# Performance work log

Hardware: AMD Instinct MI355X
Metric: run time of the kernel (lower is better)

## Reference

```python
import jax, jax.numpy as jnp
import numpy as np

# 5x5 binomial (Gaussian) kernel, as in the swd-pytorch reference this repo vendors
_K = (np.outer([1, 4, 6, 4, 1], [1, 4, 6, 4, 1]) / 256.0).astype(np.float32)

SLICE = 7
N_DESC = 128
N_REPEAT = 128
PROJ_PER_REPEAT = 4


def _gauss_conv(x, stride):
    # depthwise 5x5 conv, padding=2, NCHW
    C = x.shape[1]
    k = jnp.broadcast_to(jnp.asarray(_K)[None, None], (C, 1, 5, 5)).astype(x.dtype)
    return jax.lax.conv_general_dilated(
        x, k, window_strides=(stride, stride), padding=[(2, 2), (2, 2)],
        dimension_numbers=('NCHW', 'OIHW', 'NCHW'), feature_group_count=C)


def _pyr_up(x):
    up = jnp.repeat(jnp.repeat(x, 2, axis=2), 2, axis=3)
    return _gauss_conv(up, 1)


def _laplacian_pyramid(x, n_pyramids):
    gauss = [x]
    for _ in range(n_pyramids):
        gauss.append(_gauss_conv(gauss[-1], 2))  # pyr_down
    lap = [gauss[i] - _pyr_up(gauss[i + 1]) for i in range(n_pyramids)]
    lap.append(gauss[-1])
    return lap


def _extract_patches(layer, rows, cols):
    # gather only the selected 7x7 patches instead of materializing the full unfold
    B, C = layer.shape[0], layer.shape[1]

    def one(r, c):
        return jax.lax.dynamic_slice(layer, (0, 0, r, c), (B, C, SLICE, SLICE))

    p = jax.vmap(one)(rows, cols)           # [n_desc, B, C, 7, 7]
    p = jnp.transpose(p, (1, 0, 2, 3, 4))   # [B, n_desc, C, 7, 7]
    mean = jnp.mean(p, axis=(0, 1, 3, 4), keepdims=True)
    std = jnp.std(p, axis=(0, 1, 3, 4), keepdims=True, ddof=1)  # torch.std is unbiased
    p = (p - mean) / (std + 1e-8)
    return p.reshape(-1, C * SLICE * SLICE)  # [B*n_desc, 147]


def _lap_swd(x, y):
    n_pyramids = int(np.rint(np.log2(x.shape[2] // 16)))
    pyr1 = _laplacian_pyramid(x, n_pyramids)
    pyr2 = _laplacian_pyramid(y, n_pyramids)
    key = jax.random.key(42)
    results = []
    for i, (l1, l2) in enumerate(zip(pyr1, pyr2)):
        H, W = l1.shape[2], l1.shape[3]
        n = (H - 6) * (W - 6)
        k_idx, k_proj = jax.random.split(jax.random.fold_in(key, i))
        idx = jax.random.permutation(k_idx, n)[:min(N_DESC, n)]
        rows, cols = idx // (W - 6), idx % (W - 6)
        p1 = _extract_patches(l1, rows, cols)
        p2 = _extract_patches(l2, rows, cols)
        D = p1.shape[1]
        # all 128 repeats x 4 projections batched into one [D, 512] matrix;
        # per-column std normalization == per-repeat normalization in the original
        rand = jax.random.normal(k_proj, (D, N_REPEAT * PROJ_PER_REPEAT), dtype=p1.dtype)
        rand = rand / jnp.std(rand, axis=0, keepdims=True, ddof=1)
        proj1 = jnp.sort(p1 @ rand, axis=0)
        proj2 = jnp.sort(p2 @ rand, axis=0)
        # mean over 128 repeats of mean(|d|) == global mean (equal group sizes)
        results.append(jnp.mean(jnp.abs(proj1 - proj2)))
    return jnp.mean(jnp.stack(results)) * 1000.0


def setup_inputs() -> dict:
    key = jax.random.key(0)
    kx, ky = jax.random.split(key)
    x = jax.random.normal(kx, (128, 3, 256, 256), dtype=jnp.float32)
    y = jax.random.normal(ky, (128, 3, 256, 256), dtype=jnp.float32)
    return {"x": x, "y": y}


def reference(x, y):
    return _lap_swd(x, y)
```

## Files before the change

### kernel.cpp

```cpp
#include <hip/hip_runtime.h>
#include <hip/hip_bf16.h>
#include <cstdint>
#include <cmath>
#include <vector>
#include <algorithm>
#include <numeric>


#define SIDX(i) ((i) ^ ((((i) >> 5) ^ ((i) >> 10)) & 31))
#define EXB 1024

typedef __attribute__((ext_vector_type(8))) short bf16x8;
typedef __attribute__((ext_vector_type(4))) float f32x4;
typedef __attribute__((ext_vector_type(4))) unsigned short us4;

struct RC { unsigned int rc[128]; };
struct Keys { uint32_t a[5]; uint32_t b[5]; };

__host__ __device__ inline void tf2x32(uint32_t k0, uint32_t k1,
                                       uint32_t x0, uint32_t x1,
                                       uint32_t& o0, uint32_t& o1) {
  uint32_t k2 = k0 ^ k1 ^ 0x1BD11BDAu;
  x0 += k0; x1 += k1;
#define TFR(r) { x0 += x1; x1 = (x1 << r) | (x1 >> (32 - r)); x1 ^= x0; }
  TFR(13) TFR(15) TFR(26) TFR(6)   x0 += k1; x1 += k2 + 1u;
  TFR(17) TFR(29) TFR(16) TFR(24)  x0 += k2; x1 += k0 + 2u;
  TFR(13) TFR(15) TFR(26) TFR(6)   x0 += k0; x1 += k1 + 3u;
  TFR(17) TFR(29) TFR(16) TFR(24)  x0 += k1; x1 += k2 + 4u;
  TFR(13) TFR(15) TFR(26) TFR(6)   x0 += k2; x1 += k0 + 5u;
#undef TFR
  o0 = x0; o1 = x1;
}

struct HostTables {
  RC rcs[5];
  uint32_t kp0[5], kp1[5];
  HostTables() {
    static const int Hs[5] = {256, 128, 64, 32, 16};
    for (int l = 0; l < 5; ++l) {
      uint32_t f0, f1;
      tf2x32(0u, 42u, 0u, (uint32_t)l, f0, f1);
      uint32_t ik0, ik1;
      tf2x32(f0, f1, 0u, 0u, ik0, ik1);
      tf2x32(f0, f1, 0u, 1u, kp0[l], kp1[l]);
      int Wm6 = Hs[l] - 6;
      int n = Wm6 * Wm6;
      int nd = n < 128 ? n : 128;
      std::vector<int> perm(n);
      std::iota(perm.begin(), perm.end(), 0);
      int rounds = (int)std::ceil(3.0 * std::log((double)n) / std::log(4294967295.0));
      uint32_t key0 = ik0, key1 = ik1;
      std::vector<uint32_t> bits(n);
      std::vector<int> ord(n), tmp(n);
      for (int r = 0; r < rounds; ++r) {
        uint32_t nk0, nk1, s0, s1;
        tf2x32(key0, key1, 0u, 0u, nk0, nk1);
        tf2x32(key0, key1, 0u, 1u, s0, s1);
        key0 = nk0; key1 = nk1;
        for (int tt = 0; tt < n; ++tt) {
          uint32_t o0, o1;
          tf2x32(s0, s1, 0u, (uint32_t)tt, o0, o1);
          bits[tt] = o0 ^ o1;
        }
        std::iota(ord.begin(), ord.end(), 0);
        std::stable_sort(ord.begin(), ord.end(),
                         [&](int A, int B) { return bits[A] < bits[B]; });
        for (int i2 = 0; i2 < n; ++i2) tmp[i2] = perm[ord[i2]];
        perm.swap(tmp);
      }
      for (int d = 0; d < 128; ++d) {
        int vv = (d < nd) ? perm[d] : 0;
        rcs[l].rc[d] = ((uint32_t)(vv / Wm6) << 16) | (uint32_t)(vv % Wm6);
      }
    }
  }
};
static const HostTables g_tbl;

__device__ inline float erfinv_f(float x) {
  float w = -log1pf(-x * x);
  float p;
  if (w < 5.0f) {
    w = w - 2.5f;
    p = 2.81022636e-08f;
    p = fmaf(p, w, 3.43273939e-07f);
    p = fmaf(p, w, -3.5233877e-06f);
    p = fmaf(p, w, -4.39150654e-06f);
    p = fmaf(p, w, 0.00021858087f);
    p = fmaf(p, w, -0.00125372503f);
    p = fmaf(p, w, -0.00417768164f);
    p = fmaf(p, w, 0.246640727f);
    p = fmaf(p, w, 1.50140941f);
  } else {
    w = sqrtf(w) - 3.0f;
    p = -0.000200214257f;
    p = fmaf(p, w, 0.000100950558f);
    p = fmaf(p, w, 0.00134934322f);
    p = fmaf(p, w, -0.00367342844f);
    p = fmaf(p, w, 0.00573950773f);
    p = fmaf(p, w, -0.0076224613f);
    p = fmaf(p, w, 0.00943887047f);
    p = fmaf(p, w, 1.00167406f);
    p = fmaf(p, w, 2.83297682f);
  }
  return p * x;
}

__device__ inline float bits_to_normal(uint32_t b) {
  union { uint32_t u; float f; } cv;
  cv.u = (b >> 9) | 0x3f800000u;
  float f = cv.f - 1.0f;
  const float lo = -0.99999994f;
  const float span = 1.0f - lo;
  float u = fmaxf(lo, __fadd_rn(__fmul_rn(f, span), lo));
  return 1.41421356237f * erfinv_f(u);
}

__device__ inline uint32_t pack_bf16x2(float v) {
  uint32_t u = __float_as_uint(v);
  uint32_t hi = (u + 0x7fffu + ((u >> 16) & 1u)) >> 16;
  float r = v - __uint_as_float(hi << 16);
  uint32_t ul = __float_as_uint(r);
  uint32_t lo = (ul + 0x7fffu + ((ul >> 16) & 1u)) >> 16;
  return hi | (lo << 16);
}


__global__ __launch_bounds__(256) void down_kernel(
    const float* __restrict__ inX, float* __restrict__ outX,
    const float* __restrict__ inY, float* __restrict__ outY,
    int H, int ltr, int lgW) {
  __shared__ __align__(16) float si[2816];
  __shared__ float hb[1408];
  int W = 1 << lgW;
  int lgWo = lgW - 1;
  int Wo = W >> 1, Ho = H >> 1;
  int TR = 1 << ltr;
  int lgnby = lgWo - ltr;
  int nby = 1 << lgnby;
  int per = 384 << lgnby;
  int bid = blockIdx.x;
  const float* in = inX; float* out = outX;
  if (bid >= per) { bid -= per; in = inY; out = outY; }
  int bc = bid >> lgnby;
  int by = bid & (nby - 1);
  int oy0 = by << ltr;
  int rows = 2 * TR + 3;
  int y0 = 2 * oy0 - 2;
  const float* src = in + (size_t)bc * H * W;
  int t = threadIdx.x;

  int nf4 = (rows << lgW) >> 2;
  for (int i = t; i < nf4; i += 256) {
    int fi = i << 2;
    int r = fi >> lgW, x = fi & (W - 1);
    int y = y0 + r;
    float4 v = (y >= 0 && y < H) ? *(const float4*)(src + ((size_t)y << lgW) + x)
                                 : make_float4(0.f, 0.f, 0.f, 0.f);
    *(float4*)(si + fi) = v;
  }
  __syncthreads();

  int nh = rows << lgWo;
  for (int i = t; i < nh; i += 256) {
    int r = i >> lgWo, ox = i & (Wo - 1);
    const float* rp = si + (r << lgW);
    int xb = 2 * ox;
    float s = 0.375f * rp[xb] + 0.25f * rp[xb + 1];
    if (ox >= 1) s += 0.0625f * rp[xb - 2] + 0.25f * rp[xb - 1];
    if (xb + 2 < W) s += 0.0625f * rp[xb + 2];
    hb[i] = s;
  }
  __syncthreads();

  int no = TR << lgWo;
  float* dst = out + (size_t)bc * Ho * Wo;
  for (int i = t; i < no; i += 256) {
    int r = i >> lgWo, ox = i & (Wo - 1);
    const float* cp = hb + ((2 * r) << lgWo) + ox;
    float s = 0.0625f * cp[0] + 0.25f * cp[Wo] + 0.375f * cp[2 * Wo] +
              0.25f * cp[3 * Wo] + 0.0625f * cp[4 * Wo];
    dst[((size_t)(oy0 + r) << lgWo) + ox] = s;
  }
}

__global__ void randgen_kernel(float* __restrict__ rnd, Keys ks,
                               float* __restrict__ misc) {
  int t = blockIdx.x * 256 + threadIdx.x;
  if (blockIdx.x == 0 && threadIdx.x < 128) misc[threadIdx.x] = 0.f;
  const int per = 75264;
  int l = t / per;
  int tt = t - l * per;
  if (l < 5) {
    uint32_t o0, o1;
    tf2x32(ks.a[l], ks.b[l], 0u, (uint32_t)tt, o0, o1);
    rnd[l * per + tt] = bits_to_normal(o0 ^ o1);
  }
}

__global__ void rndstats_kernel(const float* __restrict__ rnd,
                                float* __restrict__ inv1s,
                                float* __restrict__ scS) {
  int t = blockIdx.x * 256 + threadIdx.x;
  int l = t >> 9, j = t & 511;
  const float* rp = rnd + (size_t)l * 75264 + j;
  float sum = 0.f, q = 0.f;
  float sc[3];
#pragma unroll
  for (int c = 0; c < 3; ++c) {
    float s = 0.f;
    for (int ff = 0; ff < 49; ++ff) {
      float v = rp[(c * 49 + ff) * 512];
      s += v; q = fmaf(v, v, q);
    }
    sc[c] = s; sum += s;
  }
  float mean = sum * (1.f / 147.f);
  float var = (q - 147.f * mean * mean) * (1.f / 146.f);
  inv1s[t] = 1.f / sqrtf(var);
#pragma unroll
  for (int c = 0; c < 3; ++c) scS[(size_t)l * 1536 + c * 512 + j] = sc[c];
}

template <int PAR>
__device__ __forceinline__ void lap7(
    const float* __restrict__ gc, const float (&q0)[6], const float (&q1)[6],
    const float (&q2)[6], int cb, int H, float rw0, float rw2,
    uint32_t* __restrict__ po, float& sum7, float& sq7) {
#pragma unroll
  for (int v = 0; v < 7; ++v) {
    const int iw = ((v + PAR) >> 1) + 1;
    const int xo = PAR ^ (v & 1);
    int x = cb + v;
    float val = gc[x];
    float cw0 = (x >= 2) ? (xo ? 0.0625f : 0.3125f) : 0.f;
    float cw2 = (x <= H - 3) ? (xo ? 0.3125f : 0.0625f) : 0.f;
    float s0 = cw0 * q0[iw - 1] + 0.625f * q0[iw] + cw2 * q0[iw + 1];
    float s1 = cw0 * q1[iw - 1] + 0.625f * q1[iw] + cw2 * q1[iw + 1];
    float s2 = cw0 * q2[iw - 1] + 0.625f * q2[iw] + cw2 * q2[iw + 1];
    val -= rw0 * s0 + 0.625f * s1 + rw2 * s2;
    po[v] = pack_bf16x2(val);
    sum7 += val; sq7 = fmaf(val, val, sq7);
  }
}

__global__ __launch_bounds__(256) void extract_kernel(
    const float* __restrict__ g1, const float* __restrict__ gn1,
    uint32_t* __restrict__ p1g, float* __restrict__ part1,
    const float* __restrict__ g2, const float* __restrict__ gn2,
    uint32_t* __restrict__ p2g, float* __restrict__ part2,
    RC rcs, int H, int nd, int useLap, int M) {
  __shared__ float ls[6];
  if (threadIdx.x < 6) ls[threadIdx.x] = 0.f;
  __syncthreads();
  int half = (blockIdx.x >= EXB) ? 1 : 0;
  int bid = blockIdx.x - half * EXB;
  const float* g = half ? g2 : g1;
  const float* gn = half ? gn2 : gn1;
  uint32_t* p = half ? p2g : p1g;
  float* part = half ? part2 : part1;
  int totalU = M * 22;
  for (int unit = bid * 256 + threadIdx.x; unit < totalU; unit += EXB * 256) {
    int row = unit / 22;
    int k = unit - row * 22;
    if (k < 21) {
      int d, b;
      if (nd == 128) { d = row & 127; b = row >> 7; }
      else { b = row / nd; d = row - b * nd; }
      unsigned rc = rcs.rc[d];
      int r = (int)(rc >> 16);
      int cb = (int)(rc & 0xffffu);
      int c = k / 7, u = k - (k / 7) * 7;
      int y = r + u;
      const float* gc = g + ((size_t)(b * 3 + c)) * H * H + (size_t)y * H;
      uint32_t* po = p + (size_t)row * 160 + c * 49 + u * 7;
      float sum7 = 0.f, sq7 = 0.f;
      if (useLap) {
        int H2 = H >> 1;
        const float* gnc = gn + ((size_t)(b * 3 + c)) * H2 * H2;
        int h = y >> 1, yo = y & 1;
        float rw0 = (y >= 2) ? (yo ? 0.0625f : 0.3125f) : 0.f;
        float rw2 = (y <= H - 3) ? (yo ? 0.3125f : 0.0625f) : 0.f;
        int r0 = max(h - 1, 0), r2 = min(h + 1, H2 - 1);
        const float* R0 = gnc + (size_t)r0 * H2;
        const float* R1 = gnc + (size_t)h * H2;
        const float* R2 = gnc + (size_t)r2 * H2;
        int wb = (cb >> 1) - 1;
        float q0[6], q1[6], q2[6];
#pragma unroll
        for (int kk = 0; kk < 6; ++kk) {
          int a = wb + kk;
          a = a < 0 ? 0 : (a > H2 - 1 ? H2 - 1 : a);
          q0[kk] = R0[a]; q1[kk] = R1[a]; q2[kk] = R2[a];
        }
        if (cb & 1) lap7<1>(gc, q0, q1, q2, cb, H, rw0, rw2, po, sum7, sq7);
        else        lap7<0>(gc, q0, q1, q2, cb, H, rw0, rw2, po, sum7, sq7);
      } else {
#pragma unroll
        for (int v = 0; v < 7; ++v) {
          float val = gc[cb + v];
          po[v] = pack_bf16x2(val);
          sum7 += val; sq7 = fmaf(val, val, sq7);
        }
      }
      atomicAdd(&ls[c], sum7);
      atomicAdd(&ls[3 + c], sq7);
    } else {
      uint32_t* po = p + (size_t)row * 160 + 147;
      po[0] = 0x3F80u; po[1] = 0x3F80u; po[2] = 0x3F80u;
#pragma unroll
      for (int kk = 3; kk < 13; ++kk) po[kk] = 0u;
    }
  }
  __syncthreads();
  if (threadIdx.x < 6) part[bid * 6 + threadIdx.x] = ls[threadIdx.x];
}

__global__ void redpart_kernel(const float* __restrict__ part1,
                               const float* __restrict__ part2,
                               float* __restrict__ redg) {
  __shared__ float red[12];
  int tid = threadIdx.x;
  if (tid < 12) red[tid] = 0.f;
  __syncthreads();
  if (tid < 192) {
    int k = tid >> 4, r0 = tid & 15;
    const float* src = (k < 6) ? part1 : part2;
    int kk = (k < 6) ? k : k - 6;
    float ssum = 0.f;
    for (int r = r0; r < EXB; r += 16) ssum += src[r * 6 + kk];
    atomicAdd(&red[k], ssum);
  }
  __syncthreads();
  if (tid < 12) redg[tid] = red[tid];
}

__global__ void prep_kernel(
    const float* __restrict__ rnd, const float* __restrict__ inv1v,
    const float* __restrict__ scS, const float* __restrict__ redg,
    uint32_t* __restrict__ Bt1, uint32_t* __restrict__ Bt2, float Np) {
  int j = blockIdx.x;
  int f = threadIdx.x;
  if (f >= 160) return;
  int o = j * 160 + f;
  if (f >= 150) { Bt1[o] = 0u; Bt2[o] = 0u; return; }
  int c = (f < 147) ? (f / 49) : (f - 147);
  float m1 = redg[c] / Np;
  float v1 = (redg[3 + c] - Np * m1 * m1) / (Np - 1.f);
  float i1 = 1.f / (sqrtf(fmaxf(v1, 0.f)) + 1e-8f);
  float m2 = redg[6 + c] / Np;
  float v2 = (redg[9 + c] - Np * m2 * m2) / (Np - 1.f);
  float i2 = 1.f / (sqrtf(fmaxf(v2, 0.f)) + 1e-8f);
  float inv1 = inv1v[j];
  float w1, w2;
  if (f < 147) {
    float rv = rnd[f * 512 + j] * inv1;
    w1 = rv * i1; w2 = rv * i2;
  } else {
    float s = scS[c * 512 + j] * inv1;
    w1 = -m1 * i1 * s; w2 = -m2 * i2 * s;
  }
  Bt1[o] = pack_bf16x2(w1);
  Bt2[o] = pack_bf16x2(w2);
}

#define GBM 128
#define GBN 128
__global__ __launch_bounds__(256, 3) void gemm_kernel(
    const uint32_t* __restrict__ A1, const uint32_t* __restrict__ Bt1,
    const uint32_t* __restrict__ A2, const uint32_t* __restrict__ Bt2,
    float* __restrict__ C1, float* __restrict__ C2, int M) {
  __shared__ __align__(16) unsigned short AhS[128 * 40];
  __shared__ __align__(16) unsigned short AlS[128 * 40];
  __shared__ __align__(16) unsigned short BhS[128 * 40];
  __shared__ __align__(16) unsigned short BlS[128 * 40];
  int z = blockIdx.z;
  const uint32_t* A = z ? A2 : A1;
  const uint32_t* Bt = z ? Bt2 : Bt1;
  float* C = z ? C2 : C1;
  int bm = blockIdx.x * GBM;
  int bn = blockIdx.y * GBN;
  int tid = threadIdx.x;
  int lane = tid & 63;
  int wid = tid >> 6;
  int wm = wid & 1, wn = wid >> 1;
  int fr = lane & 15;
  int kb = (lane >> 4) << 3;
  f32x4 acc[4][4];
#pragma unroll
  for (int i = 0; i < 4; ++i)
#pragma unroll
    for (int j = 0; j < 4; ++j) acc[i][j] = (f32x4){0.f, 0.f, 0.f, 0.f};

  for (int k0 = 0; k0 < 160; k0 += 32) {
#pragma unroll
    for (int i = 0; i < 4; ++i) {
      int e = tid * 16 + i * 4;
      int m = e >> 5, kk = e & 31;
      uint4 v = *(const uint4*)(A + (size_t)(bm + m) * 160 + k0 + kk);
      us4 h = {(unsigned short)v.x, (unsigned short)v.y,
               (unsigned short)v.z, (unsigned short)v.w};
      us4 l = {(unsigned short)(v.x >> 16), (unsigned short)(v.y >> 16),
               (unsigned short)(v.z >> 16), (unsigned short)(v.w >> 16)};
      *(us4*)(AhS + m * 40 + kk) = h;
      *(us4*)(AlS + m * 40 + kk) = l;
      uint4 w = *(const uint4*)(Bt + (size_t)(bn + m) * 160 + k0 + kk);
      us4 wh = {(unsigned short)w.x, (unsigned short)w.y,
                (unsigned short)w.z, (unsigned short)w.w};
      us4 wl = {(unsigned short)(w.x >> 16), (unsigned short)(w.y >> 16),
                (unsigned short)(w.z >> 16), (unsigned short)(w.w >> 16)};
      *(us4*)(BhS + m * 40 + kk) = wh;
      *(us4*)(BlS + m * 40 + kk) = wl;
    }
    __syncthreads();
    bf16x8 ah[4], al[4], bh[4], bl[4];
#pragma unroll
    for (int mt = 0; mt < 4; ++mt) {
      int m = wm * 64 + mt * 16 + fr;
      ah[mt] = *(const bf16x8*)(AhS + m * 40 + kb);
      al[mt] = *(const bf16x8*)(AlS + m * 40 + kb);
    }
#pragma unroll
    for (int nt = 0; nt < 4; ++nt) {
      int n = wn * 64 + nt * 16 + fr;
      bh[nt] = *(const bf16x8*)(BhS + n * 40 + kb);
      bl[nt] = *(const bf16x8*)(BlS + n * 40 + kb);
    }
#pragma unroll
    for (int mt = 0; mt < 4; ++mt)
#pragma unroll
      for (int nt = 0; nt < 4; ++nt) {
        acc[mt][nt] = __builtin_amdgcn_mfma_f32_16x16x32_bf16(
            ah[mt], bh[nt], acc[mt][nt], 0, 0, 0);
        acc[mt][nt] = __builtin_amdgcn_mfma_f32_16x16x32_bf16(
            ah[mt], bl[nt], acc[mt][nt], 0, 0, 0);
        acc[mt][nt] = __builtin_amdgcn_mfma_f32_16x16x32_bf16(
            al[mt], bh[nt], acc[mt][nt], 0, 0, 0);
      }
    __syncthreads();
  }
  int mrow = (lane >> 4) << 2;
#pragma unroll
  for (int mt = 0; mt < 4; ++mt)
#pragma unroll
    for (int nt = 0; nt < 4; ++nt) {
      int n = bn + wn * 64 + nt * 16 + fr;
      int m = bm + wm * 64 + mt * 16 + mrow;
      f32x4 v = acc[mt][nt];
      *(float4*)(C + (size_t)n * 16384 + m) = make_float4(v[0], v[1], v[2], v[3]);
    }
}

__device__ inline int corank(const float* __restrict__ s, int pb, int L, int so) {
  int lo = so - L; lo = lo < 0 ? 0 : lo;
  int hi = so < L ? so : L;
  while (lo < hi) {
    int mid = (lo + hi) >> 1;
    float a = s[SIDX(pb + mid)];
    float b = s[SIDX(pb + L + so - 1 - mid)];
    if (a < b) lo = mid + 1; else hi = mid;
  }
  return lo;
}

__device__ __forceinline__ void merge_round(float (&v)[32], float* __restrict__ s,
                                            int t, int bi, int L, bool crosswave) {
  int sw = ((bi >> 5) ^ (bi >> 10)) & 31;
#pragma unroll
  for (int q = 0; q < 32; ++q) s[(bi + q) ^ sw] = v[q];
  if (crosswave) __syncthreads();
  else __builtin_amdgcn_wave_barrier();
  int pb = bi & ~(2 * L - 1);
  int so = bi - pb;
  int i0 = corank(s, pb, L, so);
  int nxt = __shfl_down(i0, 1, 64);
  int i1;
  if (((so + 32) & (2 * L - 1)) == 0) i1 = L;
  else if (crosswave && (t & 63) == 63) i1 = corank(s, pb, L, so + 32);
  else i1 = nxt;
  int na = i1 - i0;
  int j1 = so + 32 - i1;
#pragma unroll
  for (int q = 0; q < 32; ++q) {
    int idx = (q < na) ? (pb + i0 + q)
                       : (pb + L + j1 - 1 - (q - na));
    v[q] = s[SIDX(idx)];
  }
#pragma unroll
  for (int j = 16; j >= 1; j >>= 1) {
#pragma unroll
    for (int q = 0; q < 32; ++q) {
      if ((q & j) == 0) {
        float a = v[q], b = v[q | j];
        v[q] = fminf(a, b);
        v[q | j] = fmaxf(a, b);
      }
    }
  }
  if (crosswave) __syncthreads();
}

__device__ __forceinline__ void mergesort_col(float (&v)[32], float* __restrict__ s,
                                              int t, int bi) {
  for (int L = 32; L <= 1024; L <<= 1) merge_round(v, s, t, bi, L, false);
  for (int L = 2048; L <= 8192; L <<= 1) merge_round(v, s, t, bi, L, true);
}

__global__ __launch_bounds__(512, 4) void sortdiff_kernel(
    const float* __restrict__ proj1, const float* __restrict__ proj2,
    float* __restrict__ sum, int m) {
  __shared__ float s[16384];
  int t = threadIdx.x;
  int col = blockIdx.x;
  const float INF = __builtin_huge_valf();
  float va[32], vb[32];
  int bi = t << 5;

  const float* pa = proj1 + (size_t)col * 16384;
  const float* pbp = proj2 + (size_t)col * 16384;
  if (bi < m) {
#pragma unroll
    for (int i = 0; i < 8; ++i) {
      float4 A4 = *(const float4*)(pa + bi + i * 4);
      va[i * 4 + 0] = A4.x; va[i * 4 + 1] = A4.y;
      va[i * 4 + 2] = A4.z; va[i * 4 + 3] = A4.w;
      float4 B4 = *(const float4*)(pbp + bi + i * 4);
      vb[i * 4 + 0] = B4.x; vb[i * 4 + 1] = B4.y;
      vb[i * 4 + 2] = B4.z; vb[i * 4 + 3] = B4.w;
    }
  } else {
#pragma unroll
    for (int r = 0; r < 32; ++r) { va[r] = INF; vb[r] = INF; }
  }

#pragma unroll
  for (int k = 2; k <= 32; k <<= 1) {
#pragma unroll
    for (int j = k >> 1; j >= 1; j >>= 1) {
#pragma unroll
      for (int r = 0; r < 32; ++r) {
        if ((r & j) == 0) {
          bool up = ((r & k) == 0);
          float a0 = va[r], b0 = va[r | j];
          float lo0 = fminf(a0, b0), hi0 = fmaxf(a0, b0);
          va[r] = up ? lo0 : hi0;
          va[r | j] = up ? hi0 : lo0;
          float a1 = vb[r], b1 = vb[r | j];
          float lo1 = fminf(a1, b1), hi1 = fmaxf(a1, b1);
          vb[r] = up ? lo1 : hi1;
          vb[r | j] = up ? hi1 : lo1;
        }
      }
    }
  }

  mergesort_col(va, s, t, bi);
  mergesort_col(vb, s, t, bi);

  float acc = 0.f;
  if (bi < m) {
#pragma unroll
    for (int q = 0; q < 32; ++q) acc += fabsf(va[q] - vb[q]);
  }

#pragma unroll
  for (int o = 32; o > 0; o >>= 1) acc += __shfl_down(acc, o, 64);
  if ((t & 63) == 0) s[t >> 6] = acc;
  __syncthreads();
  if (t == 0) {
    float tot = 0.f;
    for (int i = 0; i < 8; ++i) tot += s[i];
    atomicAdd(sum, tot);
  }
}

__global__ void final_kernel(const float* __restrict__ sums, float* __restrict__ out) {
  float r = sums[0] * (1.f / 8388608.f) + sums[1] * (1.f / 8388608.f) +
            sums[2] * (1.f / 8388608.f) + sums[3] * (1.f / 8388608.f) +
            sums[4] * (1.f / 6553600.f);
  out[0] = r * (1000.f / 5.f);
}


extern "C" void kernel_launch(void* const* d_in, const int* in_sizes, int n_in,
                              void* d_out, int out_size, void* d_ws, size_t ws_size,
                              hipStream_t stream) {
  const float* xin = (const float*)d_in[0];
  const float* yin = (const float*)d_in[1];
  float* out = (float*)d_out;

  char* base = (char*)d_ws;
  size_t off = 0;
  auto alloc = [&](size_t nfloats) -> float* {
    float* p = (float*)(base + off);
    off += ((nfloats * 4) + 255) & ~(size_t)255;
    return p;
  };
  float* gX[5];
  float* gY[5];
  gX[0] = (float*)xin;
  gY[0] = (float*)yin;
  gX[1] = alloc(6291456); gX[2] = alloc(1572864); gX[3] = alloc(393216); gX[4] = alloc(98304);
  gY[1] = alloc(6291456); gY[2] = alloc(1572864); gY[3] = alloc(393216); gY[4] = alloc(98304);
  uint32_t* p1 = (uint32_t*)alloc((size_t)16384 * 160);
  uint32_t* p2 = (uint32_t*)alloc((size_t)16384 * 160);
  float* rnd = alloc((size_t)5 * 75264);
  float* inv1s = alloc(5 * 512);
  float* scS = alloc((size_t)5 * 1536);
  float* redg = alloc(16);
  uint32_t* Bt1 = (uint32_t*)alloc(160 * 512);
  uint32_t* Bt2 = (uint32_t*)alloc(160 * 512);
  float* proj1 = alloc((size_t)16384 * 512);
  float* proj2 = alloc((size_t)16384 * 512);
  float* part1 = alloc(EXB * 6);
  float* part2 = alloc(EXB * 6);
  float* misc = alloc(128);

  static const int Hs[5] = {256, 128, 64, 32, 16};

  Keys ks;
  for (int l = 0; l < 5; ++l) { ks.a[l] = g_tbl.kp0[l]; ks.b[l] = g_tbl.kp1[l]; }
  randgen_kernel<<<1470, 256, 0, stream>>>(rnd, ks, misc);
  rndstats_kernel<<<10, 256, 0, stream>>>(rnd, inv1s, scS);

  down_kernel<<<2 * 384 * 32, 256, 0, stream>>>(xin, gX[1], yin, gY[1], 256, 2, 8);
  down_kernel<<<2 * 384 * 8, 256, 0, stream>>>(gX[1], gX[2], gY[1], gY[2], 128, 3, 7);
  down_kernel<<<2 * 384 * 2, 256, 0, stream>>>(gX[2], gX[3], gY[2], gY[3], 64, 4, 6);
  down_kernel<<<2 * 384 * 1, 256, 0, stream>>>(gX[3], gX[4], gY[3], gY[4], 32, 4, 5);

  for (int l = 0; l < 5; ++l) {
    int H = Hs[l];
    int Wm6 = H - 6;
    int n = Wm6 * Wm6;
    int nd = n < 128 ? n : 128;
    int M = 128 * nd;
    extract_kernel<<<2 * EXB, 256, 0, stream>>>(
        gX[l], (l < 4) ? gX[l + 1] : nullptr, p1, part1,
        gY[l], (l < 4) ? gY[l + 1] : nullptr, p2, part2,
        g_tbl.rcs[l], H, nd, (l < 4) ? 1 : 0, M);
    redpart_kernel<<<1, 256, 0, stream>>>(part1, part2, redg);
    prep_kernel<<<512, 192, 0, stream>>>(rnd + (size_t)l * 75264, inv1s + l * 512,
                                         scS + (size_t)l * 1536, redg, Bt1, Bt2,
                                         (float)M * 49.f);
    dim3 gg(M / 128, 4, 2);
    gemm_kernel<<<gg, 256, 0, stream>>>(p1, Bt1, p2, Bt2, proj1, proj2, M);
    sortdiff_kernel<<<512, 512, 0, stream>>>(proj1, proj2, misc + l, M);
  }
  final_kernel<<<1, 1, 0, stream>>>(misc, out);
}
```

Baseline: 1.233 ms.

## Fuse partial-sum reduction into extract via last-block counter, hoist pad writes

The separate redpart kernel launch per pyramid level is removed. The last extract block to finish, detected through an atomic counter with thread fences, now reduces the per-block partial sums into redg. The constant padding columns of the patch matrices are written once in extra randgen blocks instead of on every level, and the extract grid is enlarged from 1024 to 1344 blocks per half. This trades five small kernel launches and repeated pad stores for atomics, fences and a serial tail reduction in one block.

```diff
diff --git a/kernel.cpp b/kernel.cpp
--- a/kernel.cpp
+++ b/kernel.cpp
@@ -8,7 +8,7 @@
 
 
 #define SIDX(i) ((i) ^ ((((i) >> 5) ^ ((i) >> 10)) & 31))
-#define EXB 1024
+#define EXB 1344
 
 typedef __attribute__((ext_vector_type(8))) short bf16x8;
 typedef __attribute__((ext_vector_type(4))) float f32x4;
@@ -185,9 +185,26 @@
 }
 
 __global__ void randgen_kernel(float* __restrict__ rnd, Keys ks,
-                               float* __restrict__ misc) {
-  int t = blockIdx.x * 256 + threadIdx.x;
-  if (blockIdx.x == 0 && threadIdx.x < 128) misc[threadIdx.x] = 0.f;
+                               float* __restrict__ misc,
+                               uint32_t* __restrict__ ctr,
+                               uint32_t* __restrict__ p1,
+                               uint32_t* __restrict__ p2) {
+  int b = blockIdx.x;
+  if (b >= 1470) {
+    int u = (b - 1470) * 256 + threadIdx.x;
+    uint32_t* p = (u & 1) ? p2 : p1;
+    int row = u >> 1;
+    uint32_t* po = p + (size_t)row * 160 + 147;
+    po[0] = 0x3F80u; po[1] = 0x3F80u; po[2] = 0x3F80u;
+#pragma unroll
+    for (int kk = 3; kk < 13; ++kk) po[kk] = 0u;
+    return;
+  }
+  if (b == 0) {
+    if (threadIdx.x < 128) misc[threadIdx.x] = 0.f;
+    else if (threadIdx.x < 136) ctr[threadIdx.x - 128] = 0u;
+  }
+  int t = b * 256 + threadIdx.x;
   const int per = 75264;
   int l = t / per;
   int tt = t - l * per;
@@ -249,8 +266,10 @@
     uint32_t* __restrict__ p1g, float* __restrict__ part1,
     const float* __restrict__ g2, const float* __restrict__ gn2,
     uint32_t* __restrict__ p2g, float* __restrict__ part2,
-    RC rcs, int H, int nd, int useLap, int M) {
+    RC rcs, int H, int nd, int useLap, int M,
+    uint32_t* __restrict__ ctr, float* __restrict__ redg) {
   __shared__ float ls[6];
+  __shared__ int lastf;
   if (threadIdx.x < 6) ls[threadIdx.x] = 0.f;
   __syncthreads();
   int half = (blockIdx.x >= EXB) ? 1 : 0;
@@ -259,80 +278,75 @@
   const float* gn = half ? gn2 : gn1;
   uint32_t* p = half ? p2g : p1g;
   float* part = half ? part2 : part1;
-  int totalU = M * 22;
+  int totalU = M * 21;
   for (int unit = bid * 256 + threadIdx.x; unit < totalU; unit += EXB * 256) {
-    int row = unit / 22;
-    int k = unit - row * 22;
-    if (k < 21) {
-      int d, b;
-      if (nd == 128) { d = row & 127; b = row >> 7; }
-      else { b = row / nd; d = row - b * nd; }
-      unsigned rc = rcs.rc[d];
-      int r = (int)(rc >> 16);
-      int cb = (int)(rc & 0xffffu);
-      int c = k / 7, u = k - (k / 7) * 7;
-      int y = r + u;
-      const float* gc = g + ((size_t)(b * 3 + c)) * H * H + (size_t)y * H;
-      uint32_t* po = p + (size_t)row * 160 + c * 49 + u * 7;
-      float sum7 = 0.f, sq7 = 0.f;
-      if (useLap) {
-        int H2 = H >> 1;
-        const float* gnc = gn + ((size_t)(b * 3 + c)) * H2 * H2;
-        int h = y >> 1, yo = y & 1;
-        float rw0 = (y >= 2) ? (yo ? 0.0625f : 0.3125f) : 0.f;
-        float rw2 = (y <= H - 3) ? (yo ? 0.3125f : 0.0625f) : 0.f;
-        int r0 = max(h - 1, 0), r2 = min(h + 1, H2 - 1);
-        const float* R0 = gnc + (size_t)r0 * H2;
-        const float* R1 = gnc + (size_t)h * H2;
-        const float* R2 = gnc + (size_t)r2 * H2;
-        int wb = (cb >> 1) - 1;
-        float q0[6], q1[6], q2[6];
-#pragma unroll
-        for (int kk = 0; kk < 6; ++kk) {
-          int a = wb + kk;
-          a = a < 0 ? 0 : (a > H2 - 1 ? H2 - 1 : a);
-          q0[kk] = R0[a]; q1[kk] = R1[a]; q2[kk] = R2[a];
-        }
-        if (cb & 1) lap7<1>(gc, q0, q1, q2, cb, H, rw0, rw2, po, sum7, sq7);
-        else        lap7<0>(gc, q0, q1, q2, cb, H, rw0, rw2, po, sum7, sq7);
-      } else {
-#pragma unroll
-        for (int v = 0; v < 7; ++v) {
-          float val = gc[cb + v];
-          po[v] = pack_bf16x2(val);
-          sum7 += val; sq7 = fmaf(val, val, sq7);
-        }
+    int row = unit / 21;
+    int k = unit - row * 21;
+    int d, b;
+    if (nd == 128) { d = row & 127; b = row >> 7; }
+    else { b = row / nd; d = row - b * nd; }
+    unsigned rc = rcs.rc[d];
+    int r = (int)(rc >> 16);
+    int cb = (int)(rc & 0xffffu);
+    int c = k / 7, u = k - (k / 7) * 7;
+    int y = r + u;
+    const float* gc = g + ((size_t)(b * 3 + c)) * H * H + (size_t)y * H;
+    uint32_t* po = p + (size_t)row * 160 + c * 49 + u * 7;
+    float sum7 = 0.f, sq7 = 0.f;
+    if (useLap) {
+      int H2 = H >> 1;
+      const float* gnc = gn + ((size_t)(b * 3 + c)) * H2 * H2;
+      int h = y >> 1, yo = y & 1;
+      float rw0 = (y >= 2) ? (yo ? 0.0625f : 0.3125f) : 0.f;
+      float rw2 = (y <= H - 3) ? (yo ? 0.3125f : 0.0625f) : 0.f;
+      int r0 = max(h - 1, 0), r2 = min(h + 1, H2 - 1);
+      const float* R0 = gnc + (size_t)r0 * H2;
+      const float* R1 = gnc + (size_t)h * H2;
+      const float* R2 = gnc + (size_t)r2 * H2;
+      int wb = (cb >> 1) - 1;
+      float q0[6], q1[6], q2[6];
+#pragma unroll
+      for (int kk = 0; kk < 6; ++kk) {
+        int a = wb + kk;
+        a = a < 0 ? 0 : (a > H2 - 1 ? H2 - 1 : a);
+        q0[kk] = R0[a]; q1[kk] = R1[a]; q2[kk] = R2[a];
       }
-      atomicAdd(&ls[c], sum7);
-      atomicAdd(&ls[3 + c], sq7);
+      if (cb & 1) lap7<1>(gc, q0, q1, q2, cb, H, rw0, rw2, po, sum7, sq7);
+      else        lap7<0>(gc, q0, q1, q2, cb, H, rw0, rw2, po, sum7, sq7);
     } else {
-      uint32_t* po = p + (size_t)row * 160 + 147;
-      po[0] = 0x3F80u; po[1] = 0x3F80u; po[2] = 0x3F80u;
-#pragma unroll
-      for (int kk = 3; kk < 13; ++kk) po[kk] = 0u;
-    }
+#pragma unroll
+      for (int v = 0; v < 7; ++v) {
+        float val = gc[cb + v];
+        po[v] = pack_bf16x2(val);
+        sum7 += val; sq7 = fmaf(val, val, sq7);
+      }
+    }
+    atomicAdd(&ls[c], sum7);
+    atomicAdd(&ls[3 + c], sq7);
   }
   __syncthreads();
   if (threadIdx.x < 6) part[bid * 6 + threadIdx.x] = ls[threadIdx.x];
-}
-
-__global__ void redpart_kernel(const float* __restrict__ part1,
-                               const float* __restrict__ part2,
-                               float* __restrict__ redg) {
-  __shared__ float red[12];
-  int tid = threadIdx.x;
-  if (tid < 12) red[tid] = 0.f;
+  if (threadIdx.x == 0) {
+    __threadfence();
+    lastf = (atomicAdd(ctr, 1u) == 2 * EXB - 1) ? 1 : 0;
+  }
   __syncthreads();
-  if (tid < 192) {
-    int k = tid >> 4, r0 = tid & 15;
-    const float* src = (k < 6) ? part1 : part2;
-    int kk = (k < 6) ? k : k - 6;
-    float ssum = 0.f;
-    for (int r = r0; r < EXB; r += 16) ssum += src[r * 6 + kk];
-    atomicAdd(&red[k], ssum);
-  }
-  __syncthreads();
-  if (tid < 12) redg[tid] = red[tid];
+  if (lastf) {
+    __threadfence();
+    __shared__ float red[12];
+    if (threadIdx.x < 12) red[threadIdx.x] = 0.f;
+    __syncthreads();
+    if (threadIdx.x < 192) {
+      int k2 = threadIdx.x >> 4, r0 = threadIdx.x & 15;
+      const float* src = (k2 < 6) ? part1 : part2;
+      int kk = (k2 < 6) ? k2 : k2 - 6;
+      float ssum = 0.f;
+      for (int r = r0; r < EXB; r += 16) ssum += src[r * 6 + kk];
+      atomicAdd(&red[k2], ssum);
+    }
+    __syncthreads();
+    if (threadIdx.x < 12) redg[threadIdx.x] = red[threadIdx.x];
+  }
 }
 
 __global__ void prep_kernel(
@@ -608,6 +622,7 @@
   float* inv1s = alloc(5 * 512);
   float* scS = alloc((size_t)5 * 1536);
   float* redg = alloc(16);
+  uint32_t* ctr = (uint32_t*)alloc(8);
   uint32_t* Bt1 = (uint32_t*)alloc(160 * 512);
   uint32_t* Bt2 = (uint32_t*)alloc(160 * 512);
   float* proj1 = alloc((size_t)16384 * 512);
@@ -620,7 +635,7 @@
 
   Keys ks;
   for (int l = 0; l < 5; ++l) { ks.a[l] = g_tbl.kp0[l]; ks.b[l] = g_tbl.kp1[l]; }
-  randgen_kernel<<<1470, 256, 0, stream>>>(rnd, ks, misc);
+  randgen_kernel<<<1598, 256, 0, stream>>>(rnd, ks, misc, ctr, p1, p2);
   rndstats_kernel<<<10, 256, 0, stream>>>(rnd, inv1s, scS);
 
   down_kernel<<<2 * 384 * 32, 256, 0, stream>>>(xin, gX[1], yin, gY[1], 256, 2, 8);
@@ -637,8 +652,7 @@
     extract_kernel<<<2 * EXB, 256, 0, stream>>>(
         gX[l], (l < 4) ? gX[l + 1] : nullptr, p1, part1,
         gY[l], (l < 4) ? gY[l + 1] : nullptr, p2, part2,
-        g_tbl.rcs[l], H, nd, (l < 4) ? 1 : 0, M);
-    redpart_kernel<<<1, 256, 0, stream>>>(part1, part2, redg);
+        g_tbl.rcs[l], H, nd, (l < 4) ? 1 : 0, M, ctr + l, redg);
     prep_kernel<<<512, 192, 0, stream>>>(rnd + (size_t)l * 75264, inv1s + l * 512,
                                          scS + (size_t)l * 1536, redg, Bt1, Bt2,
                                          (float)M * 49.f);
```

After: 1.755 ms. +42.4%, slower.
